# Kernel tuning notes

Hardware: AMD Instinct MI355X
Metric: run time of the kernel (lower is better)

## Reference

```python
import jax, jax.numpy as jnp
import numpy as np

B, N, D = 8, 1024, 768
H = 3
DCAT = 2 * D          # 1536, input dim at layer 1
DK = DCAT // H        # 512
CONV_OUT = D - 2      # 766 (kernel 3, VALID)


def setup_inputs() -> dict:
    key = jax.random.key(0)
    ks = jax.random.split(key, 20)
    s = 0.02
    return {
        "adj": jax.random.uniform(ks[0], (B, N, N), dtype=jnp.float32),
        "inputs": jax.random.normal(ks[1], (B, N, D), dtype=jnp.float32),
        "score_mask": jax.random.randint(ks[2], (B, H, N, N), 0, 2).astype(bool),
        # GCN layer weights (stored [in,out]; math = torch Linear)
        "W0_w": jax.random.normal(ks[3], (D, D), dtype=jnp.float32) * s,
        "W0_b": jnp.zeros((D,), dtype=jnp.float32),
        "W1_w": jax.random.normal(ks[4], (DCAT, D), dtype=jnp.float32) * s,
        "W1_b": jnp.zeros((D,), dtype=jnp.float32),
        # MultiHeadAttention(3, 1536) query/key projections
        "q_w": jax.random.normal(ks[5], (DCAT, DCAT), dtype=jnp.float32) * s,
        "q_b": jnp.zeros((DCAT,), dtype=jnp.float32),
        "k_w": jax.random.normal(ks[6], (DCAT, DCAT), dtype=jnp.float32) * s,
        "k_b": jnp.zeros((DCAT,), dtype=jnp.float32),
        # Conv1d(n, n, 3) created in forward: OIH layout
        "conv_w": jax.random.normal(ks[7], (N, N, 3), dtype=jnp.float32) * s,
        "conv_b": jnp.zeros((N,), dtype=jnp.float32),
        # linearc: 766 -> 768
        "linc_w": jax.random.normal(ks[8], (CONV_OUT, D), dtype=jnp.float32) * s,
        "linc_b": jnp.zeros((D,), dtype=jnp.float32),
        # fc: Linear(768,768,no bias) -> ReLU -> Linear(768,768,no bias)
        "fc1_w": jax.random.normal(ks[9], (D, D), dtype=jnp.float32) * s,
        "fc2_w": jax.random.normal(ks[10], (D, D), dtype=jnp.float32) * s,
    }


def _gcn_layer(adj, x, denom, Ww, Wb):
    Ax = adj @ x                       # [B,n,din]
    AxW = (Ax @ Ww + Wb) / denom       # [B,n,768]
    return jax.nn.relu(AxW) + (x @ Ww + Wb)


def _select_top2(m):
    # per-batch top-2 threshold over flattened NxN, symmetrize, diag=1
    b, n, _ = m.shape
    flat = m.reshape(b, -1)
    thr = jax.lax.top_k(flat, 2)[0][:, -1]                  # [b]
    mask = (flat >= thr[:, None]).astype(m.dtype).reshape(b, n, n)
    mask = mask + jnp.swapaxes(mask, -1, -2)
    eye = jnp.eye(n, dtype=m.dtype)
    return mask * (1.0 - eye) + eye


def reference(adj, inputs, score_mask, W0_w, W0_b, W1_w, W1_b,
              q_w, q_b, k_w, k_b, conv_w, conv_b, linc_w, linc_b,
              fc1_w, fc2_w):
    b, n, d = inputs.shape
    # ---- layer 0 ----
    denom = adj.sum(2, keepdims=True) + 1.0
    out = _gcn_layer(adj, inputs, denom, W0_w, W0_b)        # [B,n,768]
    # Conv1d over feature axis with channels = n, VALID, k=3 -> [B,n,766]
    conve = jax.nn.relu(
        jax.lax.conv_general_dilated(out, conv_w, (1,), 'VALID',
                                     dimension_numbers=('NCH', 'OIH', 'NCH'))
        + conv_b[None, :, None])
    out = conve @ linc_w + linc_b                           # [B,n,768]
    # ---- layer 1 (semantic path) ----
    x = jnp.concatenate([inputs, out], axis=-1)             # [B,n,1536]
    h, dk = H, x.shape[-1] // H
    q = (x @ q_w + q_b).reshape(b, n, h, dk).transpose(0, 2, 1, 3)
    k = (x @ k_w + k_b).reshape(b, n, h, dk).transpose(0, 2, 1, 3)
    scores = jnp.einsum('bhqd,bhkd->bhqk', q, k) / jnp.sqrt(jnp.float32(dk))
    scores = jnp.where(score_mask, jnp.float32(-1e9), scores)
    keep = (~score_mask[:, :, :, 0:1]).astype(scores.dtype)
    attn = jax.nn.softmax(scores, axis=-1) * keep           # [B,3,n,n]
    # attention-driven head selection (softmax over batch dim, argmax over heads)
    prob = jax.nn.softmax(attn.sum((-2, -1)), axis=0)       # [B,3]
    max_idx = jnp.argmax(prob, axis=1)                      # [B]
    adj2 = jnp.take_along_axis(attn, max_idx[:, None, None, None], axis=1)[:, 0]
    adj2 = _select_top2(adj2) * adj2
    denom2 = adj2.sum(2, keepdims=True) + 1.0
    out = _gcn_layer(adj2, x, denom2, W1_w, W1_b)
    out = jax.nn.relu(out @ fc1_w) @ fc2_w
    return out
```

## Files before the change

### kernel.cpp

```cpp
#include <hip/hip_runtime.h>
#include <cstdint>
#include <cstddef>

typedef __bf16 bf16;
typedef __bf16 bf16x8 __attribute__((ext_vector_type(8)));
typedef float f32x4 __attribute__((ext_vector_type(4)));

#define B_ 8
#define N_ 1024
#define D_ 768
#define H_ 3
#define DC_ 1536
#define DK_ 512
#define PC_ 766
#define MB_ (1024ull*1024ull)

static const size_t O_DEN   = 0;
static const size_t O_DEN2  = 32768;
static const size_t O_ADIAG = 65536;
static const size_t O_T2P   = 98304;
static const size_t O_THR   = 163840;
static const size_t O_CNTS  = 164096;
static const size_t O_HSEL  = 164352;
static const size_t O_SELC  = 164608;
static const size_t O_FLAG  = 164864;
static const size_t O_QKB   = 165120;
static const size_t O_SEL   = 180224;
static const size_t O_ATTN  = 262144;
static const size_t O_X     = O_ATTN + 32*MB_;
static const size_t O_AX2   = O_X    + 24*MB_;
static const size_t O_ADJB  = O_AX2  + 24*MB_;
static const size_t O_INT   = O_ADJB + 16*MB_;
static const size_t O_BBA   = O_INT  + 12*MB_;
static const size_t O_BBB   = O_BBA  + 12*MB_;
static const size_t O_BBC   = O_BBB  + 12*MB_;
static const size_t O_W0T   = O_BBC  + 12*MB_;
static const size_t O_W1T   = O_W0T + 1179648;
static const size_t O_QKWT  = O_W1T + 2359296;
static const size_t O_CWB   = O_QKWT + 9437184;
static const size_t O_LCT   = O_CWB + 6291456;
static const size_t O_F1T   = O_LCT + 1179648;
static const size_t O_F2T   = O_F1T + 1179648;
static const size_t WS_NEED = O_F2T + 1179648;
static const size_t O_OUT0T = O_INT;

__device__ __forceinline__ bool mask_at(const void* p, int flag, size_t i) {
    switch (flag) {
        case 1:  return ((const int*)p)[i] != 0;
        case 2:  return ((const float*)p)[i] != 0.0f;
        case 3:  return ((const long long*)p)[i] != 0;
        default: return ((const unsigned char*)p)[i] != 0;
    }
}

__device__ __forceinline__ void gload16(const void* g, void* l) {
    __builtin_amdgcn_global_load_lds(
        (const __attribute__((address_space(1))) void*)g,
        (__attribute__((address_space(3))) void*)l, 16, 0, 0);
}

__device__ inline float blockMax256(float v) {
    __shared__ float red[4];
    for (int off = 32; off; off >>= 1) v = fmaxf(v, __shfl_xor(v, off));
    int lane = threadIdx.x & 63, wid = threadIdx.x >> 6;
    if (lane == 0) red[wid] = v;
    __syncthreads();
    v = fmaxf(fmaxf(red[0], red[1]), fmaxf(red[2], red[3]));
    __syncthreads();
    return v;
}

__device__ inline float blockSum256(float v) {
    __shared__ float red[4];
    for (int off = 32; off; off >>= 1) v += __shfl_xor(v, off);
    int lane = threadIdx.x & 63, wid = threadIdx.x >> 6;
    if (lane == 0) red[wid] = v;
    __syncthreads();
    v = red[0] + red[1] + red[2] + red[3];
    __syncthreads();
    return v;
}

template<int EPI>
__global__ __launch_bounds__(256) void mm(
    const bf16* __restrict__ A, size_t sA, int lda,
    const bf16* __restrict__ Bt, size_t sB, int ldb,
    const int* __restrict__ rowIdx, int rowMul,
    const float* __restrict__ bias,
    const bf16* __restrict__ Dadd, int ldd,
    const float* __restrict__ denv,
    const void* __restrict__ smask, const int* __restrict__ flagp,
    bf16* __restrict__ Cb, float* __restrict__ Cf, size_t sC, int ldc,
    int M, int N, int K)
{
    __shared__ __align__(16) bf16 As[2][64 * 32];
    __shared__ __align__(16) bf16 Bs[2][128 * 32];

    const int gx = gridDim.x, gy = gridDim.y;
    const int nwg = gx * gy * (int)gridDim.z;
    int lin = ((int)blockIdx.z * gy + (int)blockIdx.y) * gx + (int)blockIdx.x;
    int cpx = nwg >> 3;
    int swz = (lin & 7) * cpx + (lin >> 3);
    int ty = swz % gy;
    int tt = swz / gy;
    int tx = tt % gx;
    int b  = tt / gx;

    const int bm = ty * 64, bn = tx * 128;
    const int tid = threadIdx.x;
    const int lane = tid & 63, w = tid >> 6;
    const int wr = w >> 1, wc = w & 1;
    const int boff = rowIdx ? rowIdx[b] * rowMul : 0;

    const bf16* Ab = A + (size_t)b * sA;
    const bf16* Bb = Bt + (size_t)b * sB;

    const int sr = lane >> 2;
    const int sc = (lane & 3) * 8;

    f32x4 zero = {0.f, 0.f, 0.f, 0.f};
    f32x4 acc[2][4];
    #pragma unroll
    for (int i = 0; i < 2; ++i)
        #pragma unroll
        for (int j = 0; j < 4; ++j) acc[i][j] = zero;

    gload16((const void*)(Ab + (size_t)(bm + w * 16 + sr) * lda + sc),
            (void*)(As[0] + (w * 16) * 32));
    gload16((const void*)(Bb + (size_t)(boff + bn + w * 32 + sr) * ldb + sc),
            (void*)(Bs[0] + (w * 32) * 32));
    gload16((const void*)(Bb + (size_t)(boff + bn + w * 32 + 16 + sr) * ldb + sc),
            (void*)(Bs[0] + (w * 32 + 16) * 32));
    __syncthreads();

    int cur = 0;
    for (int k0 = 0; k0 < K; k0 += 32) {
        int nxt = cur ^ 1;
        if (k0 + 32 < K) {
            gload16((const void*)(Ab + (size_t)(bm + w * 16 + sr) * lda + k0 + 32 + sc),
                    (void*)(As[nxt] + (w * 16) * 32));
            gload16((const void*)(Bb + (size_t)(boff + bn + w * 32 + sr) * ldb + k0 + 32 + sc),
                    (void*)(Bs[nxt] + (w * 32) * 32));
            gload16((const void*)(Bb + (size_t)(boff + bn + w * 32 + 16 + sr) * ldb + k0 + 32 + sc),
                    (void*)(Bs[nxt] + (w * 32 + 16) * 32));
        }
        bf16x8 af[2], bfv[4];
        #pragma unroll
        for (int i = 0; i < 2; ++i)
            af[i]  = *(const bf16x8*)(As[cur] + (wr * 32 + i * 16 + (lane & 15)) * 32 + (lane >> 4) * 8);
        #pragma unroll
        for (int j = 0; j < 4; ++j)
            bfv[j] = *(const bf16x8*)(Bs[cur] + (wc * 64 + j * 16 + (lane & 15)) * 32 + (lane >> 4) * 8);
        #pragma unroll
        for (int i = 0; i < 2; ++i)
            #pragma unroll
            for (int j = 0; j < 4; ++j)
                acc[i][j] = __builtin_amdgcn_mfma_f32_16x16x32_bf16(af[i], bfv[j], acc[i][j], 0, 0, 0);
        __syncthreads();
        cur = nxt;
    }

    const int r0 = (lane >> 4) * 4, c0 = lane & 15;
    int flag = 0, h0 = 0;
    if (EPI == 4) { flag = flagp[0]; h0 = rowIdx[b]; }
    #pragma unroll
    for (int i = 0; i < 2; ++i) {
        #pragma unroll
        for (int r = 0; r < 4; ++r) {
            int m = bm + wr * 32 + i * 16 + r0 + r;
            #pragma unroll
            for (int j = 0; j < 4; ++j) {
                int n = bn + wc * 64 + j * 16 + c0;
                float v = acc[i][j][r];
                size_t oidx = (size_t)b * sC + (size_t)m * ldc + n;
                if (EPI == 0) {
                    Cb[oidx] = (bf16)(v + bias[boff + n]);
                } else if (EPI == 1) {
                    v = fmaxf((v + bias[n]) / denv[(size_t)b * M + m], 0.f)
                        + (float)Dadd[((size_t)b * M + m) * ldd + n];
                    Cb[oidx] = (bf16)v;
                } else if (EPI == 2) {
                    Cb[oidx] = (bf16)fmaxf(v, 0.f);
                } else if (EPI == 3) {
                    Cf[oidx] = v;
                } else if (EPI == 4) {
                    size_t mi = (((size_t)b * H_ + h0) * N_ + m) * N_ + n;
                    Cf[oidx] = mask_at(smask, flag, mi) ? -1e9f : v * 0.04419417382415922f;
                } else if (EPI == 5) {
                    Cb[oidx] = (n < PC_) ? (bf16)fmaxf(v + bias[m], 0.f) : (bf16)0.f;
                } else {
                    Cb[oidx] = (bf16)v;
                }
            }
        }
    }
}


__global__ __launch_bounds__(256) void k_detect(const unsigned int* __restrict__ sm,
                                                int* __restrict__ flag) {
    __shared__ int sGt1, sF32, sOddNZ;
    if (threadIdx.x == 0) { sGt1 = 0; sF32 = 0; sOddNZ = 0; }
    __syncthreads();
    int gt1 = 0, f32c = 0, oddnz = 0;
    for (int s = 0; s < 16; ++s) {
        int idx = s * 256 + threadIdx.x;
        unsigned wv = sm[idx];
        if (wv > 1u) gt1 = 1;
        if (wv == 0x3F800000u) f32c++;
        if ((idx & 1) && wv != 0u) oddnz = 1;
    }
    if (gt1)   atomicOr(&sGt1, 1);
    if (f32c)  atomicAdd(&sF32, f32c);
    if (oddnz) atomicOr(&sOddNZ, 1);
    __syncthreads();
    if (threadIdx.x == 0) {
        int f;
        if (sF32 > 512) f = 2;
        else if (!sGt1) f = sOddNZ ? 1 : 3;
        else f = 0;
        flag[0] = f;
    }
}

__global__ __launch_bounds__(256) void k_cvt_adj(const float* __restrict__ adj,
                                                 bf16* __restrict__ adjb,
                                                 float* __restrict__ den) {
    int b = blockIdx.y, row = blockIdx.x;
    size_t base = ((size_t)b * N_ + row) * N_;
    float4 v = ((const float4*)(adj + base))[threadIdx.x];
    union { bf16 b[4]; uint2 u; } o;
    o.b[0] = (bf16)v.x; o.b[1] = (bf16)v.y; o.b[2] = (bf16)v.z; o.b[3] = (bf16)v.w;
    ((uint2*)(adjb + base))[threadIdx.x] = o.u;
    float s = blockSum256(v.x + v.y + v.z + v.w);
    if (threadIdx.x == 0) den[b * N_ + row] = s + 1.0f;
}

__global__ __launch_bounds__(256) void k_cvtrows(const float* __restrict__ s,
                                                 bf16* __restrict__ d) {
    int row = blockIdx.x, t = threadIdx.x;
    if (t >= 192) return;
    float4 v = ((const float4*)(s + (size_t)row * D_))[t];
    union { bf16 b[4]; uint2 u; } o;
    o.b[0] = (bf16)v.x; o.b[1] = (bf16)v.y; o.b[2] = (bf16)v.z; o.b[3] = (bf16)v.w;
    *(uint2*)(d + (size_t)row * DC_ + t * 4) = o.u;
}

__global__ __launch_bounds__(256) void k_cw2(const float* __restrict__ w,
                                             bf16* __restrict__ d) {
    int o = blockIdx.x;
    const float* s = w + (size_t)o * 3072;
    bf16* dp = d + (size_t)o * 3072;
    for (int q = 0; q < 4; ++q) {
        int i = q * 256 + threadIdx.x;
        float v0 = s[i * 3], v1 = s[i * 3 + 1], v2 = s[i * 3 + 2];
        dp[i] = (bf16)v0; dp[1024 + i] = (bf16)v1; dp[2048 + i] = (bf16)v2;
    }
}

__global__ __launch_bounds__(256) void k_qkb(const float* __restrict__ qb,
                                             const float* __restrict__ kb,
                                             float* __restrict__ d) {
    int idx = blockIdx.x * 256 + threadIdx.x;
    if (idx >= 3072) return;
    int h = idx >> 10, rem = idx & 1023, s = rem >> 9, r = rem & 511;
    d[idx] = (s ? kb : qb)[h * 512 + r];
}

__global__ __launch_bounds__(256) void k_trcvt(
    const float* __restrict__ src, bf16* __restrict__ dst,
    int R, int C, int Rpad, int Cpad, size_t sSrc, size_t sDst, int mode)
{
    __shared__ float t[32][33];
    int b = blockIdx.z;
    int r0 = blockIdx.y * 32, c0 = blockIdx.x * 32;
    int tx = threadIdx.x & 31, ty = threadIdx.x >> 5;
    const float* s = src + (size_t)b * sSrc;
    bf16* d = dst + (size_t)b * sDst;
    #pragma unroll
    for (int q = 0; q < 4; ++q) {
        int r = r0 + ty + q * 8, c = c0 + tx;
        t[ty + q * 8][tx] = (r < R && c < C) ? s[(size_t)r * C + c] : 0.f;
    }
    __syncthreads();
    #pragma unroll
    for (int q = 0; q < 4; ++q) {
        int dr = c0 + ty + q * 8, dc = r0 + tx;
        if (dr < Cpad && dc < Rpad) {
            int drm = dr;
            if (mode == 1) drm = (dr >> 9) * 1024 + (dr & 511);
            else if (mode == 2) drm = (dr >> 9) * 1024 + 512 + (dr & 511);
            d[(size_t)drm * Rpad + dc] = (bf16)t[tx][ty + q * 8];
        }
    }
}

__global__ __launch_bounds__(256) void k_tr_bf16(const bf16* __restrict__ src,
                                                 bf16* __restrict__ dst) {
    __shared__ bf16 t[32][34];
    int b = blockIdx.z;
    int i0 = blockIdx.y * 32, p0 = blockIdx.x * 32;
    int tx = threadIdx.x & 31, ty = threadIdx.x >> 5;
    const bf16* s = src + (size_t)b * N_ * D_;
    bf16* d = dst + (size_t)b * D_ * N_;
    #pragma unroll
    for (int q = 0; q < 4; ++q)
        t[ty + q * 8][tx] = s[(size_t)(i0 + ty + q * 8) * D_ + p0 + tx];
    __syncthreads();
    #pragma unroll
    for (int q = 0; q < 4; ++q)
        d[(size_t)(p0 + ty + q * 8) * N_ + i0 + tx] = t[tx][ty + q * 8];
}

__global__ __launch_bounds__(256) void k_softmax(float* __restrict__ Sc,
                                                 const void* __restrict__ smask,
                                                 const int* __restrict__ flagp,
                                                 const int* __restrict__ hsel,
                                                 float* __restrict__ part) {
    __shared__ float s1[256], s2[256];
    int b = blockIdx.y, row = blockIdx.x;
    int h0 = hsel[b], flag = flagp[0];
    float* rp = Sc + ((size_t)b * N_ + row) * N_;
    float v[4];
    float mx = -INFINITY;
    #pragma unroll
    for (int s = 0; s < 4; ++s) { v[s] = rp[s * 256 + threadIdx.x]; mx = fmaxf(mx, v[s]); }
    mx = blockMax256(mx);
    float sum = 0.f;
    #pragma unroll
    for (int s = 0; s < 4; ++s) { v[s] = expf(v[s] - mx); sum += v[s]; }
    sum = blockSum256(sum);
    size_t ki = (((size_t)b * H_ + h0) * N_ + row) * N_;
    float keep = mask_at(smask, flag, ki) ? 0.f : 1.f;
    float inv = keep / sum;
    float m1 = -INFINITY, m2 = -INFINITY;
    #pragma unroll
    for (int s = 0; s < 4; ++s) {
        float x = v[s] * inv;
        rp[s * 256 + threadIdx.x] = x;
        if (x > m1) { m2 = m1; m1 = x; } else m2 = fmaxf(m2, x);
    }
    int tid = threadIdx.x;
    s1[tid] = m1; s2[tid] = m2;
    __syncthreads();
    for (int off = 128; off; off >>= 1) {
        if (tid < off) {
            float a1 = s1[tid], a2 = s2[tid], b1 = s1[tid + off], b2 = s2[tid + off];
            s1[tid] = fmaxf(a1, b1);
            s2[tid] = fmaxf(fminf(a1, b1), fmaxf(a2, b2));
        }
        __syncthreads();
    }
    if (tid == 0) {
        part[((size_t)b * N_ + row) * 2]     = s1[0];
        part[((size_t)b * N_ + row) * 2 + 1] = s2[0];
    }
}

__global__ __launch_bounds__(256) void k_count(const void* __restrict__ smask,
                                               const int* __restrict__ flagp,
                                               int* __restrict__ counts) {
    int bh = blockIdx.x, flag = flagp[0];
    float c = 0.f;
    for (int s = 0; s < 4; ++s) {
        int q = s * 256 + threadIdx.x;
        size_t mi = ((size_t)bh * N_ + q) * N_;
        if (!mask_at(smask, flag, mi)) c += 1.f;
    }
    c = blockSum256(c);
    if (threadIdx.x == 0) counts[bh] = (int)(c + 0.5f);
}

__global__ void k_select_head(const int* __restrict__ counts, int* __restrict__ hsel) {
    if (threadIdx.x != 0 || blockIdx.x != 0) return;
    float p[B_][H_];
    for (int h = 0; h < H_; ++h) {
        float mx = -1e30f;
        for (int b = 0; b < B_; ++b) mx = fmaxf(mx, (float)counts[b * H_ + h]);
        float s = 0.f;
        for (int b = 0; b < B_; ++b) { p[b][h] = expf((float)counts[b * H_ + h] - mx); s += p[b][h]; }
        for (int b = 0; b < B_; ++b) p[b][h] /= s;
    }
    for (int b = 0; b < B_; ++b) {
        int best = 0; float bv = p[b][0];
        for (int h = 1; h < H_; ++h) if (p[b][h] > bv) { bv = p[b][h]; best = h; }
        hsel[b] = best;
    }
}

__global__ void k_zero_sel(int* __restrict__ selcnt) {
    if (threadIdx.x < B_) selcnt[threadIdx.x] = 0;
}

__global__ __launch_bounds__(256) void k_top2_s2(const float* __restrict__ part,
                                                 float* __restrict__ thr) {
    __shared__ float s1[256], s2[256];
    int b = blockIdx.x, tid = threadIdx.x;
    float m1 = -INFINITY, m2 = -INFINITY;
    for (int s = 0; s < 4; ++s) {
        int r = s * 256 + tid;
        float a1 = part[((size_t)b * N_ + r) * 2];
        float a2 = part[((size_t)b * N_ + r) * 2 + 1];
        float n1 = fmaxf(m1, a1);
        float n2 = fmaxf(fminf(m1, a1), fmaxf(m2, a2));
        m1 = n1; m2 = n2;
    }
    s1[tid] = m1; s2[tid] = m2;
    __syncthreads();
    for (int off = 128; off; off >>= 1) {
        if (tid < off) {
            float a1 = s1[tid], a2 = s2[tid], b1 = s1[tid + off], b2 = s2[tid + off];
            s1[tid] = fmaxf(a1, b1);
            s2[tid] = fmaxf(fminf(a1, b1), fmaxf(a2, b2));
        }
        __syncthreads();
    }
    if (tid == 0) thr[b] = s2[0];
}

__global__ __launch_bounds__(256) void k_extract(const float* __restrict__ attn,
                                                 const float* __restrict__ thr,
                                                 int* __restrict__ selcnt,
                                                 int* __restrict__ sel) {
    int b = blockIdx.y;
    const float* ap = attn + (size_t)b * N_ * N_;
    float t = thr[b];
    size_t base = (size_t)blockIdx.x * 1024;
    for (int s = 0; s < 4; ++s) {
        size_t e = base + s * 256 + threadIdx.x;
        float v = ap[e];
        if (v >= t) {
            int pos = atomicAdd(&selcnt[b], 1);
            if (pos < 512) {
                sel[((size_t)b * 512 + pos) * 2]     = (int)(e >> 10);
                sel[((size_t)b * 512 + pos) * 2 + 1] = (int)(e & 1023);
            }
        }
    }
}

__global__ __launch_bounds__(256) void k_diag(const float* __restrict__ attn,
                                              float* __restrict__ adiag,
                                              float* __restrict__ den2) {
    int i = blockIdx.x * 256 + threadIdx.x;
    int b = i >> 10, r = i & 1023;
    float v = attn[(((size_t)b * N_) + r) * N_ + r];
    adiag[i] = v;
    den2[i] = v + 1.0f;
}

__global__ __launch_bounds__(256) void k_ax2_init(const bf16* __restrict__ x,
                                                  const float* __restrict__ adiag,
                                                  bf16* __restrict__ ax2) {
    int row = blockIdx.x;
    float a = adiag[row];
    const bf16* xp = x + (size_t)row * DC_;
    bf16* op = ax2 + (size_t)row * DC_;
    for (int s = 0; s < 6; ++s) {
        int d = s * 256 + threadIdx.x;
        op[d] = (bf16)(a * (float)xp[d]);
    }
}

__global__ __launch_bounds__(256) void k_ax2_sparse(const float* __restrict__ attn,
                                                    const bf16* __restrict__ x,
                                                    const int* __restrict__ selcnt,
                                                    const int* __restrict__ sel,
                                                    bf16* __restrict__ ax2,
                                                    float* __restrict__ den2) {
    int b = blockIdx.x;
    int cnt = selcnt[b]; if (cnt > 512) cnt = 512;
    __shared__ int si[1024];
    if (threadIdx.x == 0) {
        for (int e = 0; e < cnt; ++e) {
            si[e * 2]     = sel[((size_t)b * 512 + e) * 2];
            si[e * 2 + 1] = sel[((size_t)b * 512 + e) * 2 + 1];
        }
        for (int a = 1; a < cnt; ++a) {
            int ii = si[a * 2], jj = si[a * 2 + 1];
            long long key = (long long)ii * N_ + jj;
            int p = a - 1;
            while (p >= 0 && ((long long)si[p * 2] * N_ + si[p * 2 + 1]) > key) {
                si[(p + 1) * 2] = si[p * 2]; si[(p + 1) * 2 + 1] = si[p * 2 + 1]; --p;
            }
            si[(p + 1) * 2] = ii; si[(p + 1) * 2 + 1] = jj;
        }
    }
    __syncthreads();
    const float* ap = attn + (size_t)b * N_ * N_;
    for (int e = 0; e < cnt; ++e) {
        int i = si[e * 2], j = si[e * 2 + 1];
        if (i == j) continue;
        float aij = ap[(size_t)i * N_ + j];
        float aji = ap[(size_t)j * N_ + i];
        bf16* ri = ax2 + ((size_t)b * N_ + i) * DC_;
        bf16* rj = ax2 + ((size_t)b * N_ + j) * DC_;
        const bf16* xi = x + ((size_t)b * N_ + i) * DC_;
        const bf16* xj = x + ((size_t)b * N_ + j) * DC_;
        for (int s = 0; s < 6; ++s) {
            int d = s * 256 + threadIdx.x;
            ri[d] = (bf16)((float)ri[d] + aij * (float)xj[d]);
            rj[d] = (bf16)((float)rj[d] + aji * (float)xi[d]);
        }
        if (threadIdx.x == 0) {
            den2[b * N_ + i] += aij;
            den2[b * N_ + j] += aji;
        }
        __syncthreads();
    }
}

extern "C" void kernel_launch(void* const* d_in, const int* in_sizes, int n_in,
                              void* d_out, int out_size, void* d_ws, size_t ws_size,
                              hipStream_t stream) {
    if (n_in < 17) return;
    if (ws_size < WS_NEED) return;

    const float* adj    = (const float*)d_in[0];
    const float* inputs = (const float*)d_in[1];
    const void*  smask  = d_in[2];
    const float* W0w = (const float*)d_in[3];
    const float* W0b = (const float*)d_in[4];
    const float* W1w = (const float*)d_in[5];
    const float* W1b = (const float*)d_in[6];
    const float* qw  = (const float*)d_in[7];
    const float* qb  = (const float*)d_in[8];
    const float* kw  = (const float*)d_in[9];
    const float* kb  = (const float*)d_in[10];
    const float* convw = (const float*)d_in[11];
    const float* convb = (const float*)d_in[12];
    const float* lincw = (const float*)d_in[13];
    const float* lincb = (const float*)d_in[14];
    const float* fc1w  = (const float*)d_in[15];
    const float* fc2w  = (const float*)d_in[16];

    char* W = (char*)d_ws;
    float* out = (float*)d_out;

    float* den    = (float*)(W + O_DEN);
    float* den2   = (float*)(W + O_DEN2);
    float* adiag  = (float*)(W + O_ADIAG);
    float* t2p    = (float*)(W + O_T2P);
    float* thr    = (float*)(W + O_THR);
    int*   counts = (int*)(W + O_CNTS);
    int*   hsel   = (int*)(W + O_HSEL);
    int*   selcnt = (int*)(W + O_SELC);
    int*   flag   = (int*)(W + O_FLAG);
    float* qkb    = (float*)(W + O_QKB);
    int*   sel    = (int*)(W + O_SEL);
    float* ATTN   = (float*)(W + O_ATTN);
    bf16* X     = (bf16*)(W + O_X);
    bf16* AX2   = (bf16*)(W + O_AX2);
    bf16* QKOUT = (bf16*)(W + O_AX2);
    bf16* ADJB  = (bf16*)(W + O_ADJB);
    bf16* INT_  = (bf16*)(W + O_INT);
    bf16* OUT0T = (bf16*)(W + O_OUT0T);
    bf16* BBA   = (bf16*)(W + O_BBA);
    bf16* BBB   = (bf16*)(W + O_BBB);
    bf16* BBC   = (bf16*)(W + O_BBC);
    bf16* W0T   = (bf16*)(W + O_W0T);
    bf16* W1T   = (bf16*)(W + O_W1T);
    bf16* QKWT  = (bf16*)(W + O_QKWT);
    bf16* CW2   = (bf16*)(W + O_CWB);
    bf16* LCT   = (bf16*)(W + O_LCT);
    bf16* F1T   = (bf16*)(W + O_F1T);
    bf16* F2T   = (bf16*)(W + O_F2T);

    const size_t sND  = (size_t)N_ * D_;
    const size_t sNDC = (size_t)N_ * DC_;
    const size_t sNN  = (size_t)N_ * N_;

    k_detect<<<1, 256, 0, stream>>>((const unsigned int*)smask, flag);
    k_cvt_adj<<<dim3(N_, B_), 256, 0, stream>>>(adj, ADJB, den);
    k_cvtrows<<<B_ * N_, 256, 0, stream>>>(inputs, X);
    k_cw2<<<1024, 256, 0, stream>>>(convw, CW2);
    k_qkb<<<12, 256, 0, stream>>>(qb, kb, qkb);
    k_trcvt<<<dim3(24, 32, B_), 256, 0, stream>>>(inputs, INT_, N_, D_, N_, D_, sND, sND, 0);
    k_trcvt<<<dim3(24, 24, 1), 256, 0, stream>>>(W0w, W0T, D_, D_, D_, D_, 0, 0, 0);
    k_trcvt<<<dim3(24, 48, 1), 256, 0, stream>>>(W1w, W1T, DC_, D_, DC_, D_, 0, 0, 0);
    k_trcvt<<<dim3(48, 48, 1), 256, 0, stream>>>(qw, QKWT, DC_, DC_, DC_, DC_, 0, 0, 1);
    k_trcvt<<<dim3(48, 48, 1), 256, 0, stream>>>(kw, QKWT, DC_, DC_, DC_, DC_, 0, 0, 2);
    k_trcvt<<<dim3(24, 24, 1), 256, 0, stream>>>(lincw, LCT, PC_, D_, D_, D_, 0, 0, 0);
    k_trcvt<<<dim3(24, 24, 1), 256, 0, stream>>>(fc1w, F1T, D_, D_, D_, D_, 0, 0, 0);
    k_trcvt<<<dim3(24, 24, 1), 256, 0, stream>>>(fc2w, F2T, D_, D_, D_, D_, 0, 0, 0);

    mm<0><<<dim3(6, 16, B_), 256, 0, stream>>>(X, sNDC, DC_, W0T, 0, D_, nullptr, 0,
        W0b, nullptr, 0, nullptr, nullptr, nullptr, BBA, nullptr, sND, D_, N_, D_, D_);
    mm<6><<<dim3(6, 16, B_), 256, 0, stream>>>(ADJB, sNN, N_, INT_, sND, N_, nullptr, 0,
        nullptr, nullptr, 0, nullptr, nullptr, nullptr, BBB, nullptr, sND, D_, N_, D_, N_);
    mm<1><<<dim3(6, 16, B_), 256, 0, stream>>>(BBB, sND, D_, W0T, 0, D_, nullptr, 0,
        W0b, BBA, D_, den, nullptr, nullptr, BBC, nullptr, sND, D_, N_, D_, D_);
    k_tr_bf16<<<dim3(24, 32, B_), 256, 0, stream>>>(BBC, OUT0T);
    mm<5><<<dim3(6, 16, B_), 256, 0, stream>>>(CW2, 0, 3072, OUT0T, sND, N_, nullptr, 0,
        convb, nullptr, 0, nullptr, nullptr, nullptr, BBB, nullptr, sND, D_, N_, D_, 3072);
    mm<0><<<dim3(6, 16, B_), 256, 0, stream>>>(BBB, sND, D_, LCT, 0, D_, nullptr, 0,
        lincb, nullptr, 0, nullptr, nullptr, nullptr, X + D_, nullptr, sNDC, DC_, N_, D_, D_);

    k_count<<<B_ * H_, 256, 0, stream>>>(smask, flag, counts);
    k_select_head<<<1, 64, 0, stream>>>(counts, hsel);

    mm<0><<<dim3(8, 16, B_), 256, 0, stream>>>(X, sNDC, DC_, QKWT, 0, DC_, hsel, 1024,
        qkb, nullptr, 0, nullptr, nullptr, nullptr, QKOUT, nullptr, sNN, N_, N_, N_, DC_);
    mm<4><<<dim3(8, 16, B_), 256, 0, stream>>>(QKOUT, sNN, N_, QKOUT + 512, sNN, N_, hsel, 0,
        nullptr, nullptr, 0, nullptr, smask, flag, nullptr, ATTN, sNN, N_, N_, N_, DK_);
    k_softmax<<<dim3(N_, B_), 256, 0, stream>>>(ATTN, smask, flag, hsel, t2p);

    k_zero_sel<<<1, 64, 0, stream>>>(selcnt);
    k_top2_s2<<<B_, 256, 0, stream>>>(t2p, thr);
    k_extract<<<dim3(1024, B_), 256, 0, stream>>>(ATTN, thr, selcnt, sel);
    k_diag<<<32, 256, 0, stream>>>(ATTN, adiag, den2);
    k_ax2_init<<<B_ * N_, 256, 0, stream>>>(X, adiag, AX2);
    k_ax2_sparse<<<B_, 256, 0, stream>>>(ATTN, X, selcnt, sel, AX2, den2);

    mm<0><<<dim3(6, 16, B_), 256, 0, stream>>>(X, sNDC, DC_, W1T, 0, DC_, nullptr, 0,
        W1b, nullptr, 0, nullptr, nullptr, nullptr, BBA, nullptr, sND, D_, N_, D_, DC_);
    mm<1><<<dim3(6, 16, B_), 256, 0, stream>>>(AX2, sNDC, DC_, W1T, 0, DC_, nullptr, 0,
        W1b, BBA, D_, den2, nullptr, nullptr, BBB, nullptr, sND, D_, N_, D_, DC_);

    mm<2><<<dim3(6, 16, B_), 256, 0, stream>>>(BBB, sND, D_, F1T, 0, D_, nullptr, 0,
        nullptr, nullptr, 0, nullptr, nullptr, nullptr, BBC, nullptr, sND, D_, N_, D_, D_);
    mm<3><<<dim3(6, 16, B_), 256, 0, stream>>>(BBC, sND, D_, F2T, 0, D_, nullptr, 0,
        nullptr, nullptr, 0, nullptr, nullptr, nullptr, nullptr, out, sND, D_, N_, D_, D_);
}
```

Before: 477.2 us.

## Use two waves per GEMM tile with larger per-wave outputs and XOR-swizzled LDS

The mm kernel's 64x128 tile now runs on 2 waves of 128 threads instead of 4 waves, so each wave computes a 64x64 sub-tile with 4x4 MFMA accumulators. This doubles register reuse of the A and B fragments per LDS read. The global-to-LDS copies and the fragment reads also gain a matching XOR swizzle on the k-chunk column to avoid LDS bank conflicts. In exchange there are fewer waves per workgroup to hide latency, and register pressure per thread is higher.

New measurement: 522.8 us. +9.6%, slower.

```diff
diff --git a/kernel.cpp b/kernel.cpp
--- a/kernel.cpp
+++ b/kernel.cpp
@@ -82,7 +82,7 @@
 }
 
 template<int EPI>
-__global__ __launch_bounds__(256) void mm(
+__global__ __launch_bounds__(128) void mm(
     const bf16* __restrict__ A, size_t sA, int lda,
     const bf16* __restrict__ Bt, size_t sB, int ldb,
     const int* __restrict__ rowIdx, int rowMul,
@@ -109,50 +109,55 @@
     const int bm = ty * 64, bn = tx * 128;
     const int tid = threadIdx.x;
     const int lane = tid & 63, w = tid >> 6;
-    const int wr = w >> 1, wc = w & 1;
     const int boff = rowIdx ? rowIdx[b] * rowMul : 0;
 
     const bf16* Ab = A + (size_t)b * sA;
     const bf16* Bb = Bt + (size_t)b * sB;
 
     const int sr = lane >> 2;
-    const int sc = (lane & 3) * 8;
+    const int gk = (((lane & 3) ^ ((lane >> 3) & 3))) * 8;
 
     f32x4 zero = {0.f, 0.f, 0.f, 0.f};
-    f32x4 acc[2][4];
-    #pragma unroll
-    for (int i = 0; i < 2; ++i)
+    f32x4 acc[4][4];
+    #pragma unroll
+    for (int i = 0; i < 4; ++i)
         #pragma unroll
         for (int j = 0; j < 4; ++j) acc[i][j] = zero;
 
-    gload16((const void*)(Ab + (size_t)(bm + w * 16 + sr) * lda + sc),
-            (void*)(As[0] + (w * 16) * 32));
-    gload16((const void*)(Bb + (size_t)(boff + bn + w * 32 + sr) * ldb + sc),
-            (void*)(Bs[0] + (w * 32) * 32));
-    gload16((const void*)(Bb + (size_t)(boff + bn + w * 32 + 16 + sr) * ldb + sc),
-            (void*)(Bs[0] + (w * 32 + 16) * 32));
-    __syncthreads();
+    #pragma unroll
+    for (int q = 0; q < 2; ++q)
+        gload16((const void*)(Ab + (size_t)(bm + w * 32 + q * 16 + sr) * lda + gk),
+                (void*)(As[0] + (w * 32 + q * 16) * 32));
+    #pragma unroll
+    for (int q = 0; q < 4; ++q)
+        gload16((const void*)(Bb + (size_t)(boff + bn + w * 64 + q * 16 + sr) * ldb + gk),
+                (void*)(Bs[0] + (w * 64 + q * 16) * 32));
+    __syncthreads();
+
+    const int cs = ((lane >> 4) ^ ((lane >> 1) & 3)) * 8;
+    const int rl = lane & 15;
 
     int cur = 0;
     for (int k0 = 0; k0 < K; k0 += 32) {
         int nxt = cur ^ 1;
         if (k0 + 32 < K) {
-            gload16((const void*)(Ab + (size_t)(bm + w * 16 + sr) * lda + k0 + 32 + sc),
-                    (void*)(As[nxt] + (w * 16) * 32));
-            gload16((const void*)(Bb + (size_t)(boff + bn + w * 32 + sr) * ldb + k0 + 32 + sc),
-                    (void*)(Bs[nxt] + (w * 32) * 32));
-            gload16((const void*)(Bb + (size_t)(boff + bn + w * 32 + 16 + sr) * ldb + k0 + 32 + sc),
-                    (void*)(Bs[nxt] + (w * 32 + 16) * 32));
-        }
-        bf16x8 af[2], bfv[4];
+            #pragma unroll
+            for (int q = 0; q < 2; ++q)
+                gload16((const void*)(Ab + (size_t)(bm + w * 32 + q * 16 + sr) * lda + k0 + 32 + gk),
+                        (void*)(As[nxt] + (w * 32 + q * 16) * 32));
+            #pragma unroll
+            for (int q = 0; q < 4; ++q)
+                gload16((const void*)(Bb + (size_t)(boff + bn + w * 64 + q * 16 + sr) * ldb + k0 + 32 + gk),
+                        (void*)(Bs[nxt] + (w * 64 + q * 16) * 32));
+        }
+        bf16x8 af[4], bfv[4];
         #pragma unroll
-        for (int i = 0; i < 2; ++i)
-            af[i]  = *(const bf16x8*)(As[cur] + (wr * 32 + i * 16 + (lane & 15)) * 32 + (lane >> 4) * 8);
+        for (int i = 0; i < 4; ++i) {
+            af[i]  = *(const bf16x8*)(As[cur] + (i * 16 + rl) * 32 + cs);
+            bfv[i] = *(const bf16x8*)(Bs[cur] + (w * 64 + i * 16 + rl) * 32 + cs);
+        }
         #pragma unroll
-        for (int j = 0; j < 4; ++j)
-            bfv[j] = *(const bf16x8*)(Bs[cur] + (wc * 64 + j * 16 + (lane & 15)) * 32 + (lane >> 4) * 8);
-        #pragma unroll
-        for (int i = 0; i < 2; ++i)
+        for (int i = 0; i < 4; ++i)
             #pragma unroll
             for (int j = 0; j < 4; ++j)
                 acc[i][j] = __builtin_amdgcn_mfma_f32_16x16x32_bf16(af[i], bfv[j], acc[i][j], 0, 0, 0);
@@ -164,13 +169,13 @@
     int flag = 0, h0 = 0;
     if (EPI == 4) { flag = flagp[0]; h0 = rowIdx[b]; }
     #pragma unroll
-    for (int i = 0; i < 2; ++i) {
+    for (int i = 0; i < 4; ++i) {
         #pragma unroll
         for (int r = 0; r < 4; ++r) {
-            int m = bm + wr * 32 + i * 16 + r0 + r;
+            int m = bm + i * 16 + r0 + r;
             #pragma unroll
             for (int j = 0; j < 4; ++j) {
-                int n = bn + wc * 64 + j * 16 + c0;
+                int n = bn + w * 64 + j * 16 + c0;
                 float v = acc[i][j][r];
                 size_t oidx = (size_t)b * sC + (size_t)m * ldc + n;
                 if (EPI == 0) {
@@ -584,24 +589,24 @@
     k_trcvt<<<dim3(24, 24, 1), 256, 0, stream>>>(fc1w, F1T, D_, D_, D_, D_, 0, 0, 0);
     k_trcvt<<<dim3(24, 24, 1), 256, 0, stream>>>(fc2w, F2T, D_, D_, D_, D_, 0, 0, 0);
 
-    mm<0><<<dim3(6, 16, B_), 256, 0, stream>>>(X, sNDC, DC_, W0T, 0, D_, nullptr, 0,
+    mm<0><<<dim3(6, 16, B_), 128, 0, stream>>>(X, sNDC, DC_, W0T, 0, D_, nullptr, 0,
         W0b, nullptr, 0, nullptr, nullptr, nullptr, BBA, nullptr, sND, D_, N_, D_, D_);
-    mm<6><<<dim3(6, 16, B_), 256, 0, stream>>>(ADJB, sNN, N_, INT_, sND, N_, nullptr, 0,
+    mm<6><<<dim3(6, 16, B_), 128, 0, stream>>>(ADJB, sNN, N_, INT_, sND, N_, nullptr, 0,
         nullptr, nullptr, 0, nullptr, nullptr, nullptr, BBB, nullptr, sND, D_, N_, D_, N_);
-    mm<1><<<dim3(6, 16, B_), 256, 0, stream>>>(BBB, sND, D_, W0T, 0, D_, nullptr, 0,
+    mm<1><<<dim3(6, 16, B_), 128, 0, stream>>>(BBB, sND, D_, W0T, 0, D_, nullptr, 0,
         W0b, BBA, D_, den, nullptr, nullptr, BBC, nullptr, sND, D_, N_, D_, D_);
     k_tr_bf16<<<dim3(24, 32, B_), 256, 0, stream>>>(BBC, OUT0T);
-    mm<5><<<dim3(6, 16, B_), 256, 0, stream>>>(CW2, 0, 3072, OUT0T, sND, N_, nullptr, 0,
+    mm<5><<<dim3(6, 16, B_), 128, 0, stream>>>(CW2, 0, 3072, OUT0T, sND, N_, nullptr, 0,
         convb, nullptr, 0, nullptr, nullptr, nullptr, BBB, nullptr, sND, D_, N_, D_, 3072);
-    mm<0><<<dim3(6, 16, B_), 256, 0, stream>>>(BBB, sND, D_, LCT, 0, D_, nullptr, 0,
+    mm<0><<<dim3(6, 16, B_), 128, 0, stream>>>(BBB, sND, D_, LCT, 0, D_, nullptr, 0,
         lincb, nullptr, 0, nullptr, nullptr, nullptr, X + D_, nullptr, sNDC, DC_, N_, D_, D_);
 
     k_count<<<B_ * H_, 256, 0, stream>>>(smask, flag, counts);
     k_select_head<<<1, 64, 0, stream>>>(counts, hsel);
 
-    mm<0><<<dim3(8, 16, B_), 256, 0, stream>>>(X, sNDC, DC_, QKWT, 0, DC_, hsel, 1024,
+    mm<0><<<dim3(8, 16, B_), 128, 0, stream>>>(X, sNDC, DC_, QKWT, 0, DC_, hsel, 1024,
         qkb, nullptr, 0, nullptr, nullptr, nullptr, QKOUT, nullptr, sNN, N_, N_, N_, DC_);
-    mm<4><<<dim3(8, 16, B_), 256, 0, stream>>>(QKOUT, sNN, N_, QKOUT + 512, sNN, N_, hsel, 0,
+    mm<4><<<dim3(8, 16, B_), 128, 0, stream>>>(QKOUT, sNN, N_, QKOUT + 512, sNN, N_, hsel, 0,
         nullptr, nullptr, 0, nullptr, smask, flag, nullptr, ATTN, sNN, N_, N_, N_, DK_);
     k_softmax<<<dim3(N_, B_), 256, 0, stream>>>(ATTN, smask, flag, hsel, t2p);
 
@@ -612,13 +617,13 @@
     k_ax2_init<<<B_ * N_, 256, 0, stream>>>(X, adiag, AX2);
     k_ax2_sparse<<<B_, 256, 0, stream>>>(ATTN, X, selcnt, sel, AX2, den2);
 
-    mm<0><<<dim3(6, 16, B_), 256, 0, stream>>>(X, sNDC, DC_, W1T, 0, DC_, nullptr, 0,
+    mm<0><<<dim3(6, 16, B_), 128, 0, stream>>>(X, sNDC, DC_, W1T, 0, DC_, nullptr, 0,
         W1b, nullptr, 0, nullptr, nullptr, nullptr, BBA, nullptr, sND, D_, N_, D_, DC_);
-    mm<1><<<dim3(6, 16, B_), 256, 0, stream>>>(AX2, sNDC, DC_, W1T, 0, DC_, nullptr, 0,
+    mm<1><<<dim3(6, 16, B_), 128, 0, stream>>>(AX2, sNDC, DC_, W1T, 0, DC_, nullptr, 0,
         W1b, BBA, D_, den2, nullptr, nullptr, BBB, nullptr, sND, D_, N_, D_, DC_);
 
-    mm<2><<<dim3(6, 16, B_), 256, 0, stream>>>(BBB, sND, D_, F1T, 0, D_, nullptr, 0,
+    mm<2><<<dim3(6, 16, B_), 128, 0, stream>>>(BBB, sND, D_, F1T, 0, D_, nullptr, 0,
         nullptr, nullptr, 0, nullptr, nullptr, nullptr, BBC, nullptr, sND, D_, N_, D_, D_);
-    mm<3><<<dim3(6, 16, B_), 256, 0, stream>>>(BBC, sND, D_, F2T, 0, D_, nullptr, 0,
+    mm<3><<<dim3(6, 16, B_), 128, 0, stream>>>(BBC, sND, D_, F2T, 0, D_, nullptr, 0,
         nullptr, nullptr, 0, nullptr, nullptr, nullptr, nullptr, out, sND, D_, N_, D_, D_);
 }
```

## XOR-swizzle GEMM LDS tiles and fold zeroing/diag kernels into neighbors

Applied to the files above, without the earlier changes.

The bf16 MFMA GEMM now permutes which 8-element k-chunk each lane fetches from global memory, and applies the matching XOR swizzle when reading fragments from LDS. The goal is to cut LDS bank conflicts on fragment reads in every GEMM. Separately, the selection-counter reset moves into k_top2_s2 and the diagonal/den2 extraction moves into k_extract, which removes two small kernel launches. The swizzle must stay consistent between the global→LDS copy and the fragment reads, or the results will be wrong.

Result: faster. 464.3 us (-2.7%).

```diff
diff --git a/kernel.cpp b/kernel.cpp
--- a/kernel.cpp
+++ b/kernel.cpp
@@ -116,7 +116,7 @@
     const bf16* Bb = Bt + (size_t)b * sB;
 
     const int sr = lane >> 2;
-    const int sc = (lane & 3) * 8;
+    const int gk = (((lane & 3) ^ ((lane >> 3) & 3))) * 8;
 
     f32x4 zero = {0.f, 0.f, 0.f, 0.f};
     f32x4 acc[2][4];
@@ -125,32 +125,35 @@
         #pragma unroll
         for (int j = 0; j < 4; ++j) acc[i][j] = zero;
 
-    gload16((const void*)(Ab + (size_t)(bm + w * 16 + sr) * lda + sc),
+    gload16((const void*)(Ab + (size_t)(bm + w * 16 + sr) * lda + gk),
             (void*)(As[0] + (w * 16) * 32));
-    gload16((const void*)(Bb + (size_t)(boff + bn + w * 32 + sr) * ldb + sc),
-            (void*)(Bs[0] + (w * 32) * 32));
-    gload16((const void*)(Bb + (size_t)(boff + bn + w * 32 + 16 + sr) * ldb + sc),
-            (void*)(Bs[0] + (w * 32 + 16) * 32));
-    __syncthreads();
+    #pragma unroll
+    for (int q = 0; q < 2; ++q)
+        gload16((const void*)(Bb + (size_t)(boff + bn + w * 32 + q * 16 + sr) * ldb + gk),
+                (void*)(Bs[0] + (w * 32 + q * 16) * 32));
+    __syncthreads();
+
+    const int cs = ((lane >> 4) ^ ((lane >> 1) & 3)) * 8;
+    const int rl = lane & 15;
 
     int cur = 0;
     for (int k0 = 0; k0 < K; k0 += 32) {
         int nxt = cur ^ 1;
         if (k0 + 32 < K) {
-            gload16((const void*)(Ab + (size_t)(bm + w * 16 + sr) * lda + k0 + 32 + sc),
+            gload16((const void*)(Ab + (size_t)(bm + w * 16 + sr) * lda + k0 + 32 + gk),
                     (void*)(As[nxt] + (w * 16) * 32));
-            gload16((const void*)(Bb + (size_t)(boff + bn + w * 32 + sr) * ldb + k0 + 32 + sc),
-                    (void*)(Bs[nxt] + (w * 32) * 32));
-            gload16((const void*)(Bb + (size_t)(boff + bn + w * 32 + 16 + sr) * ldb + k0 + 32 + sc),
-                    (void*)(Bs[nxt] + (w * 32 + 16) * 32));
+            #pragma unroll
+            for (int q = 0; q < 2; ++q)
+                gload16((const void*)(Bb + (size_t)(boff + bn + w * 32 + q * 16 + sr) * ldb + k0 + 32 + gk),
+                        (void*)(Bs[nxt] + (w * 32 + q * 16) * 32));
         }
         bf16x8 af[2], bfv[4];
         #pragma unroll
         for (int i = 0; i < 2; ++i)
-            af[i]  = *(const bf16x8*)(As[cur] + (wr * 32 + i * 16 + (lane & 15)) * 32 + (lane >> 4) * 8);
+            af[i]  = *(const bf16x8*)(As[cur] + (wr * 32 + i * 16 + rl) * 32 + cs);
         #pragma unroll
         for (int j = 0; j < 4; ++j)
-            bfv[j] = *(const bf16x8*)(Bs[cur] + (wc * 64 + j * 16 + (lane & 15)) * 32 + (lane >> 4) * 8);
+            bfv[j] = *(const bf16x8*)(Bs[cur] + (wc * 64 + j * 16 + rl) * 32 + cs);
         #pragma unroll
         for (int i = 0; i < 2; ++i)
             #pragma unroll
@@ -388,12 +391,9 @@
     }
 }
 
-__global__ void k_zero_sel(int* __restrict__ selcnt) {
-    if (threadIdx.x < B_) selcnt[threadIdx.x] = 0;
-}
-
 __global__ __launch_bounds__(256) void k_top2_s2(const float* __restrict__ part,
-                                                 float* __restrict__ thr) {
+                                                 float* __restrict__ thr,
+                                                 int* __restrict__ selcnt) {
     __shared__ float s1[256], s2[256];
     int b = blockIdx.x, tid = threadIdx.x;
     float m1 = -INFINITY, m2 = -INFINITY;
@@ -415,38 +415,34 @@
         }
         __syncthreads();
     }
-    if (tid == 0) thr[b] = s2[0];
+    if (tid == 0) { thr[b] = s2[0]; selcnt[b] = 0; }
 }
 
 __global__ __launch_bounds__(256) void k_extract(const float* __restrict__ attn,
                                                  const float* __restrict__ thr,
                                                  int* __restrict__ selcnt,
-                                                 int* __restrict__ sel) {
-    int b = blockIdx.y;
+                                                 int* __restrict__ sel,
+                                                 float* __restrict__ adiag,
+                                                 float* __restrict__ den2) {
+    int b = blockIdx.y, row = blockIdx.x;
     const float* ap = attn + (size_t)b * N_ * N_;
     float t = thr[b];
-    size_t base = (size_t)blockIdx.x * 1024;
+    size_t base = (size_t)row * 1024;
     for (int s = 0; s < 4; ++s) {
-        size_t e = base + s * 256 + threadIdx.x;
-        float v = ap[e];
+        int col = s * 256 + threadIdx.x;
+        float v = ap[base + col];
+        if (col == row) {
+            adiag[b * N_ + row] = v;
+            den2[b * N_ + row] = v + 1.0f;
+        }
         if (v >= t) {
             int pos = atomicAdd(&selcnt[b], 1);
             if (pos < 512) {
-                sel[((size_t)b * 512 + pos) * 2]     = (int)(e >> 10);
-                sel[((size_t)b * 512 + pos) * 2 + 1] = (int)(e & 1023);
+                sel[((size_t)b * 512 + pos) * 2]     = row;
+                sel[((size_t)b * 512 + pos) * 2 + 1] = col;
             }
         }
     }
-}
-
-__global__ __launch_bounds__(256) void k_diag(const float* __restrict__ attn,
-                                              float* __restrict__ adiag,
-                                              float* __restrict__ den2) {
-    int i = blockIdx.x * 256 + threadIdx.x;
-    int b = i >> 10, r = i & 1023;
-    float v = attn[(((size_t)b * N_) + r) * N_ + r];
-    adiag[i] = v;
-    den2[i] = v + 1.0f;
 }
 
 __global__ __launch_bounds__(256) void k_ax2_init(const bf16* __restrict__ x,
@@ -605,10 +601,8 @@
         nullptr, nullptr, 0, nullptr, smask, flag, nullptr, ATTN, sNN, N_, N_, N_, DK_);
     k_softmax<<<dim3(N_, B_), 256, 0, stream>>>(ATTN, smask, flag, hsel, t2p);
 
-    k_zero_sel<<<1, 64, 0, stream>>>(selcnt);
-    k_top2_s2<<<B_, 256, 0, stream>>>(t2p, thr);
-    k_extract<<<dim3(1024, B_), 256, 0, stream>>>(ATTN, thr, selcnt, sel);
-    k_diag<<<32, 256, 0, stream>>>(ATTN, adiag, den2);
+    k_top2_s2<<<B_, 256, 0, stream>>>(t2p, thr, selcnt);
+    k_extract<<<dim3(N_, B_), 256, 0, stream>>>(ATTN, thr, selcnt, sel, adiag, den2);
     k_ax2_init<<<B_ * N_, 256, 0, stream>>>(X, adiag, AX2);
     k_ax2_sparse<<<B_, 256, 0, stream>>>(ATTN, X, selcnt, sel, AX2, den2);
 
```
